# Kernel optimization log

Measured on AMD Instinct MI355X. Metric: run time of the kernel, lower is better.

## Reference

```python
import jax, jax.numpy as jnp
import numpy as np

B, T, F = 2048, 256, 64
EMB, UNITS = 16, 32
CAT = UNITS + EMB  # concat([h, x]) -> 48


def setup_inputs() -> dict:
    key = jax.random.key(0)
    ks = jax.random.split(key, 12)
    s = lambda k, shape, fan: jax.random.normal(k, shape, jnp.float32) / np.sqrt(fan)
    return {
        "x": jax.random.normal(ks[0], (B, T, F), jnp.float32),
        "W_emb": s(ks[1], (F, EMB), F), "b_emb": jnp.zeros((EMB,), jnp.float32),
        "W_f": s(ks[2], (CAT, UNITS), CAT), "b_f": jnp.zeros((UNITS,), jnp.float32),
        "W_i": s(ks[3], (CAT, UNITS), CAT), "b_i": jnp.zeros((UNITS,), jnp.float32),
        "W_c": s(ks[4], (CAT, UNITS), CAT), "b_c": jnp.zeros((UNITS,), jnp.float32),
        "W_o": s(ks[5], (CAT, UNITS), CAT), "b_o": jnp.zeros((UNITS,), jnp.float32),
        "W_out": s(ks[6], (UNITS, 1), UNITS), "b_out": jnp.zeros((1,), jnp.float32),
    }


def reference(x, W_emb, b_emb, W_f, b_f, W_i, b_i, W_c, b_c, W_o, b_o, W_out, b_out):
    # embedding: Dense(16, sigmoid)
    e = jax.nn.sigmoid(jnp.einsum('btf,fe->bte', x, W_emb) + b_emb)  # [B,T,EMB]
    e_t = jnp.swapaxes(e, 0, 1)  # [T,B,EMB] for scan

    h0 = jnp.zeros((x.shape[0], UNITS), jnp.float32)
    c0 = jnp.zeros((x.shape[0], UNITS), jnp.float32)

    # fuse 4 gate Dense layers into one GEMM per step (same math)
    W_gates = jnp.concatenate([W_f, W_i, W_c, W_o], axis=1)  # [CAT, 4*UNITS]
    b_gates = jnp.concatenate([b_f, b_i, b_c, b_o], axis=0)

    def step(carry, x_t):
        h, c = carry
        z = jnp.concatenate([h, x_t], axis=-1)  # concat([h_t, x_t])
        g = z @ W_gates + b_gates  # [B, 4*UNITS]
        f = jax.nn.sigmoid(g[:, :UNITS])
        i = jax.nn.sigmoid(g[:, UNITS:2 * UNITS])
        ch = jnp.tanh(g[:, 2 * UNITS:3 * UNITS])
        o = jax.nn.sigmoid(g[:, 3 * UNITS:])
        c_new = f * c + i * ch
        h_new = o * jnp.tanh(c_new)
        return (h_new, c_new), None

    (h_last, _), _ = jax.lax.scan(step, (h0, c0), e_t)
    return jax.nn.sigmoid(h_last @ W_out + b_out)  # [B,1]
```

## Files before the change

### kernel.cpp

```cpp
#include <hip/hip_runtime.h>

#define B_ 2048
#define T_ 256
#define F_ 64
#define EMB_ 16
#define UNITS_ 32
#define L2E 1.44269504f

typedef __attribute__((ext_vector_type(8))) short bf16x8;
typedef __attribute__((ext_vector_type(4))) float f32x4;

__device__ __forceinline__ unsigned short f2bf(float f) {
    unsigned u = __float_as_uint(f);
    return (unsigned short)((u + 0x7FFFu + ((u >> 16) & 1u)) >> 16);
}
__device__ __forceinline__ float fast_sigmoid(float x) {
    return __builtin_amdgcn_rcpf(1.0f + __builtin_amdgcn_exp2f(-L2E * x));
}

__global__ __launch_bounds__(64) void embed_mfma(
    const float* __restrict__ x, const float* __restrict__ Wemb,
    const float* __restrict__ bemb, unsigned int* __restrict__ e_ws)
{
    __shared__ unsigned short slab[2][16][72];

    const int lane = threadIdx.x;
    const int g = lane >> 4, c = lane & 15;
    const int tile = blockIdx.x >> 5;
    const int t0 = (blockIdx.x & 31) * 8;

    bf16x8 A1, A2;
    #pragma unroll
    for (int j = 0; j < 4; ++j) {
        A1[j]     = (short)f2bf(Wemb[(4 * g + j) * EMB_ + c]);
        A1[j + 4] = (short)f2bf(Wemb[(16 + 4 * g + j) * EMB_ + c]);
        A2[j]     = (short)f2bf(Wemb[(32 + 4 * g + j) * EMB_ + c]);
        A2[j + 4] = (short)f2bf(Wemb[(48 + 4 * g + j) * EMB_ + c]);
    }
    f32x4 bc;
    #pragma unroll
    for (int r = 0; r < 4; ++r) bc[r] = bemb[4 * g + r];

    const int sr = lane >> 2, sc = lane & 3;
    const float* xs = x + (size_t)(tile * 16 + sr) * T_ * F_ + sc * 16;

    float4 rld[4], nld[4];
    {
        const float4* p = (const float4*)(xs + (size_t)t0 * F_);
        rld[0] = p[0]; rld[1] = p[1]; rld[2] = p[2]; rld[3] = p[3];
    }

    #pragma unroll
    for (int i = 0; i < 9; ++i) {
        if (i < 7) {
            const float4* p = (const float4*)(xs + (size_t)(t0 + i + 1) * F_);
            nld[0] = p[0]; nld[1] = p[1]; nld[2] = p[2]; nld[3] = p[3];
        }
        if (i < 8) {
            const float* f = (const float*)rld;
            unsigned u[8];
            #pragma unroll
            for (int k = 0; k < 8; ++k)
                u[k] = (unsigned)f2bf(f[2 * k]) | ((unsigned)f2bf(f[2 * k + 1]) << 16);
            uint4* d = (uint4*)&slab[i & 1][sr][sc * 16];
            d[0] = make_uint4(u[0], u[1], u[2], u[3]);
            d[1] = make_uint4(u[4], u[5], u[6], u[7]);
        }
        if (i > 0) {
            const unsigned short* row = &slab[(i - 1) & 1][c][0];
            ushort4 l1 = *(const ushort4*)(row + 4 * g);
            ushort4 h1 = *(const ushort4*)(row + 16 + 4 * g);
            ushort4 l2 = *(const ushort4*)(row + 32 + 4 * g);
            ushort4 h2 = *(const ushort4*)(row + 48 + 4 * g);
            bf16x8 B1 = {(short)l1.x, (short)l1.y, (short)l1.z, (short)l1.w,
                         (short)h1.x, (short)h1.y, (short)h1.z, (short)h1.w};
            bf16x8 B2 = {(short)l2.x, (short)l2.y, (short)l2.z, (short)l2.w,
                         (short)h2.x, (short)h2.y, (short)h2.z, (short)h2.w};
            f32x4 acc = __builtin_amdgcn_mfma_f32_16x16x32_bf16(A1, B1, bc, 0, 0, 0);
            acc = __builtin_amdgcn_mfma_f32_16x16x32_bf16(A2, B2, acc, 0, 0, 0);
            unsigned u0 = (unsigned)f2bf(fast_sigmoid(acc[0])) |
                          ((unsigned)f2bf(fast_sigmoid(acc[1])) << 16);
            unsigned u1 = (unsigned)f2bf(fast_sigmoid(acc[2])) |
                          ((unsigned)f2bf(fast_sigmoid(acc[3])) << 16);
            size_t idx = (((size_t)tile * T_ + (t0 + i - 1)) * 64 + lane) * 2;
            *(uint2*)(e_ws + idx) = make_uint2(u0, u1);
        }
        #pragma unroll
        for (int k = 0; k < 4; ++k) rld[k] = nld[k];
    }
}

__global__ __launch_bounds__(256) void lstm_rec(
    const float* __restrict__ Wf, const float* __restrict__ bfv,
    const float* __restrict__ Wi, const float* __restrict__ biv,
    const float* __restrict__ Wc, const float* __restrict__ bcv,
    const float* __restrict__ Wo, const float* __restrict__ bov,
    const float* __restrict__ Wout, const float* __restrict__ bout,
    const unsigned int* __restrict__ e_ws, float* __restrict__ out)
{
    __shared__ unsigned short hx[2][16][36];
    __shared__ float pred[4][16];

    const int tid = threadIdx.x;
    const int w = tid >> 6;
    const int lane = tid & 63;
    const int g = lane >> 4, m15 = lane & 15;
    const int bt = blockIdx.x;

    const int gate = m15 & 3;
    const float* Wsel = (gate == 0) ? Wf : (gate == 1) ? Wi : (gate == 2) ? Wc : Wo;
    const float ascale = (gate == 2) ? (-2.0f * L2E) : (-L2E);
    const int uAb = 8 * w + 2 * (m15 >> 2);

    bf16x8 Ah[2], Ae[2];
    #pragma unroll
    for (int tau = 0; tau < 2; ++tau) {
        const int uA = uAb + tau;
        #pragma unroll
        for (int j = 0; j < 4; ++j) {
            Ah[tau][j]     = (short)f2bf(ascale * Wsel[(4 * g + j) * UNITS_ + uA]);
            Ah[tau][j + 4] = (short)f2bf(ascale * Wsel[(16 + 4 * g + j) * UNITS_ + uA]);
            Ae[tau][j]     = (short)f2bf(ascale * Wsel[(32 + 4 * g + j) * UNITS_ + uA]);
            Ae[tau][j + 4] = 0;
        }
    }
    f32x4 bias[2];
    #pragma unroll
    for (int tau = 0; tau < 2; ++tau) {
        const int u = 8 * w + 2 * g + tau;
        bias[tau][0] = -L2E * bfv[u];
        bias[tau][1] = -L2E * biv[u];
        bias[tau][2] = -2.0f * L2E * bcv[u];
        bias[tau][3] = -L2E * bov[u];
    }

    const uint2* ep = (const uint2*)e_ws + (size_t)bt * T_ * 64 + lane;
    uint2 ering[4];
    #pragma unroll
    for (int s = 0; s < 4; ++s) ering[s] = ep[(size_t)s * 64];

    for (int i = tid; i < 2 * 16 * 36 / 2; i += 256) ((unsigned*)hx)[i] = 0;
    __syncthreads();

    float c0 = 0.f, c1 = 0.f, hf0 = 0.f, hf1 = 0.f;

    auto cell = [&](const f32x4& acc, float& cst, float& hf) {
        float Ef = __builtin_amdgcn_exp2f(acc[0]);
        float Ei = __builtin_amdgcn_exp2f(acc[1]);
        float Ec = __builtin_amdgcn_exp2f(acc[2]);
        float Eo = __builtin_amdgcn_exp2f(acc[3]);
        float Pf = 1.f + Ef, Pi = 1.f + Ei, Pc = 1.f + Ec, Po = 1.f + Eo;
        float Mc = 1.f - Ec;
        float t1 = Pi * Pc;
        float num = fmaf(cst, t1, Pf * Mc);
        float den = Pf * t1;
        float cn = num * __builtin_amdgcn_rcpf(den);
        cst = cn;
        float Eh = __builtin_amdgcn_exp2f(cn * (-2.0f * L2E));
        float Mh = 1.f - Eh;
        float d2 = (1.f + Eh) * Po;
        hf = Mh * __builtin_amdgcn_rcpf(d2);
    };

    f32x4 Fe0, Fe1;
    {
        uint2 ev = ering[0];
        bf16x8 Be = {(short)(ev.x & 0xffff), (short)(ev.x >> 16),
                     (short)(ev.y & 0xffff), (short)(ev.y >> 16), 0, 0, 0, 0};
        Fe0 = __builtin_amdgcn_mfma_f32_16x16x32_bf16(Ae[0], Be, bias[0], 0, 0, 0);
        Fe1 = __builtin_amdgcn_mfma_f32_16x16x32_bf16(Ae[1], Be, bias[1], 0, 0, 0);
    }

    #pragma unroll 1
    for (int t = 0; t < T_; t += 4) {
        #pragma unroll
        for (int s = 0; s < 4; ++s) {
            const int u = t + s;
            const unsigned short* hrow = &hx[u & 1][m15][0];
            ushort4 hlo = *(const ushort4*)(hrow + 4 * g);
            ushort4 hhi = *(const ushort4*)(hrow + 16 + 4 * g);
            bf16x8 Bh = {(short)hlo.x, (short)hlo.y, (short)hlo.z, (short)hlo.w,
                         (short)hhi.x, (short)hhi.y, (short)hhi.z, (short)hhi.w};
            f32x4 a0 = __builtin_amdgcn_mfma_f32_16x16x32_bf16(Ah[0], Bh, Fe0, 0, 0, 0);
            f32x4 a1 = __builtin_amdgcn_mfma_f32_16x16x32_bf16(Ah[1], Bh, Fe1, 0, 0, 0);

            int tn = (u + 4 < T_) ? u + 4 : T_ - 1;
            uint2 ev = ering[(s + 1) & 3];
            ering[s] = ep[(size_t)tn * 64];
            bf16x8 Be = {(short)(ev.x & 0xffff), (short)(ev.x >> 16),
                         (short)(ev.y & 0xffff), (short)(ev.y >> 16), 0, 0, 0, 0};
            Fe0 = __builtin_amdgcn_mfma_f32_16x16x32_bf16(Ae[0], Be, bias[0], 0, 0, 0);
            Fe1 = __builtin_amdgcn_mfma_f32_16x16x32_bf16(Ae[1], Be, bias[1], 0, 0, 0);

            cell(a0, c0, hf0);
            cell(a1, c1, hf1);
            unsigned pk;
            asm("v_cvt_pk_bf16_f32 %0, %1, %2" : "=v"(pk) : "v"(hf0), "v"(hf1));
            *(unsigned*)&hx[(u + 1) & 1][m15][8 * w + 2 * g] = pk;

            asm volatile("s_waitcnt lgkmcnt(0)\n\ts_barrier" ::: "memory");
        }
    }

    float p = hf0 * Wout[8 * w + 2 * g] + hf1 * Wout[8 * w + 2 * g + 1];
    p += __shfl_xor(p, 16, 64);
    p += __shfl_xor(p, 32, 64);
    if (lane < 16) pred[w][lane] = p;
    __syncthreads();
    if (tid < 16)
        out[bt * 16 + tid] = fast_sigmoid(pred[0][tid] + pred[1][tid] +
                                          pred[2][tid] + pred[3][tid] + bout[0]);
}

extern "C" void kernel_launch(void* const* d_in, const int* in_sizes, int n_in,
                              void* d_out, int out_size, void* d_ws, size_t ws_size,
                              hipStream_t stream) {
    const float* x    = (const float*)d_in[0];
    const float* Wemb = (const float*)d_in[1];
    const float* bemb = (const float*)d_in[2];
    const float* Wf   = (const float*)d_in[3];
    const float* bfv  = (const float*)d_in[4];
    const float* Wi   = (const float*)d_in[5];
    const float* biv  = (const float*)d_in[6];
    const float* Wc   = (const float*)d_in[7];
    const float* bcv  = (const float*)d_in[8];
    const float* Wo   = (const float*)d_in[9];
    const float* bov  = (const float*)d_in[10];
    const float* Wout = (const float*)d_in[11];
    const float* bout = (const float*)d_in[12];
    float* out = (float*)d_out;
    unsigned int* e_ws = (unsigned int*)d_ws;

    hipLaunchKernelGGL(embed_mfma, dim3(128 * 32), dim3(64), 0, stream,
                       x, Wemb, bemb, e_ws);
    hipLaunchKernelGGL(lstm_rec, dim3(B_ / 16), dim3(256), 0, stream,
                       Wf, bfv, Wi, biv, Wc, bcv, Wo, bov, Wout, bout,
                       (const unsigned int*)e_ws, out);
}
```

Measured before the change: 88.37 us.

## Fuse embedding and recurrence into one kernel with per-chunk flag handoff

Merges the embedding GEMM kernel and the LSTM recurrence kernel into a single launch. The first 1024 blocks compute embedding chunks, one wave each, and publish a per-tile, per-chunk release flag. The last 128 blocks spin on those flags and consume chunks as they become ready. The goal is to overlap the recurrence with the embedding work and remove the gap between the two launches. The cost is that correctness depends on producer blocks being scheduled before or alongside consumers, which is a deadlock risk. It also relies on a magic-value flag protocol that is reset at the end, on workspace state that persists across calls, and on spin-wait overhead.

```diff
diff --git a/kernel.cpp b/kernel.cpp
--- a/kernel.cpp
+++ b/kernel.cpp
@@ -6,6 +6,7 @@
 #define EMB_ 16
 #define UNITS_ 32
 #define L2E 1.44269504f
+#define MAGIC 0x51E5C0DEu
 
 typedef __attribute__((ext_vector_type(8))) short bf16x8;
 typedef __attribute__((ext_vector_type(4))) float f32x4;
@@ -18,86 +19,18 @@
     return __builtin_amdgcn_rcpf(1.0f + __builtin_amdgcn_exp2f(-L2E * x));
 }
 
-__global__ __launch_bounds__(64) void embed_mfma(
-    const float* __restrict__ x, const float* __restrict__ Wemb,
-    const float* __restrict__ bemb, unsigned int* __restrict__ e_ws)
-{
-    __shared__ unsigned short slab[2][16][72];
-
-    const int lane = threadIdx.x;
-    const int g = lane >> 4, c = lane & 15;
-    const int tile = blockIdx.x >> 5;
-    const int t0 = (blockIdx.x & 31) * 8;
-
-    bf16x8 A1, A2;
-    #pragma unroll
-    for (int j = 0; j < 4; ++j) {
-        A1[j]     = (short)f2bf(Wemb[(4 * g + j) * EMB_ + c]);
-        A1[j + 4] = (short)f2bf(Wemb[(16 + 4 * g + j) * EMB_ + c]);
-        A2[j]     = (short)f2bf(Wemb[(32 + 4 * g + j) * EMB_ + c]);
-        A2[j + 4] = (short)f2bf(Wemb[(48 + 4 * g + j) * EMB_ + c]);
-    }
-    f32x4 bc;
-    #pragma unroll
-    for (int r = 0; r < 4; ++r) bc[r] = bemb[4 * g + r];
-
-    const int sr = lane >> 2, sc = lane & 3;
-    const float* xs = x + (size_t)(tile * 16 + sr) * T_ * F_ + sc * 16;
-
-    float4 rld[4], nld[4];
-    {
-        const float4* p = (const float4*)(xs + (size_t)t0 * F_);
-        rld[0] = p[0]; rld[1] = p[1]; rld[2] = p[2]; rld[3] = p[3];
-    }
-
-    #pragma unroll
-    for (int i = 0; i < 9; ++i) {
-        if (i < 7) {
-            const float4* p = (const float4*)(xs + (size_t)(t0 + i + 1) * F_);
-            nld[0] = p[0]; nld[1] = p[1]; nld[2] = p[2]; nld[3] = p[3];
-        }
-        if (i < 8) {
-            const float* f = (const float*)rld;
-            unsigned u[8];
-            #pragma unroll
-            for (int k = 0; k < 8; ++k)
-                u[k] = (unsigned)f2bf(f[2 * k]) | ((unsigned)f2bf(f[2 * k + 1]) << 16);
-            uint4* d = (uint4*)&slab[i & 1][sr][sc * 16];
-            d[0] = make_uint4(u[0], u[1], u[2], u[3]);
-            d[1] = make_uint4(u[4], u[5], u[6], u[7]);
-        }
-        if (i > 0) {
-            const unsigned short* row = &slab[(i - 1) & 1][c][0];
-            ushort4 l1 = *(const ushort4*)(row + 4 * g);
-            ushort4 h1 = *(const ushort4*)(row + 16 + 4 * g);
-            ushort4 l2 = *(const ushort4*)(row + 32 + 4 * g);
-            ushort4 h2 = *(const ushort4*)(row + 48 + 4 * g);
-            bf16x8 B1 = {(short)l1.x, (short)l1.y, (short)l1.z, (short)l1.w,
-                         (short)h1.x, (short)h1.y, (short)h1.z, (short)h1.w};
-            bf16x8 B2 = {(short)l2.x, (short)l2.y, (short)l2.z, (short)l2.w,
-                         (short)h2.x, (short)h2.y, (short)h2.z, (short)h2.w};
-            f32x4 acc = __builtin_amdgcn_mfma_f32_16x16x32_bf16(A1, B1, bc, 0, 0, 0);
-            acc = __builtin_amdgcn_mfma_f32_16x16x32_bf16(A2, B2, acc, 0, 0, 0);
-            unsigned u0 = (unsigned)f2bf(fast_sigmoid(acc[0])) |
-                          ((unsigned)f2bf(fast_sigmoid(acc[1])) << 16);
-            unsigned u1 = (unsigned)f2bf(fast_sigmoid(acc[2])) |
-                          ((unsigned)f2bf(fast_sigmoid(acc[3])) << 16);
-            size_t idx = (((size_t)tile * T_ + (t0 + i - 1)) * 64 + lane) * 2;
-            *(uint2*)(e_ws + idx) = make_uint2(u0, u1);
-        }
-        #pragma unroll
-        for (int k = 0; k < 4; ++k) rld[k] = nld[k];
-    }
-}
-
-__global__ __launch_bounds__(256) void lstm_rec(
+__global__ __launch_bounds__(256) void lstm_all(
+    const float* __restrict__ x,
+    const float* __restrict__ Wemb, const float* __restrict__ bemb,
     const float* __restrict__ Wf, const float* __restrict__ bfv,
     const float* __restrict__ Wi, const float* __restrict__ biv,
     const float* __restrict__ Wc, const float* __restrict__ bcv,
     const float* __restrict__ Wo, const float* __restrict__ bov,
     const float* __restrict__ Wout, const float* __restrict__ bout,
-    const unsigned int* __restrict__ e_ws, float* __restrict__ out)
+    unsigned int* __restrict__ e_ws, unsigned int* __restrict__ flags,
+    float* __restrict__ out)
 {
+    __shared__ unsigned short slab[4][2][16][72];
     __shared__ unsigned short hx[2][16][36];
     __shared__ float pred[4][16];
 
@@ -105,7 +38,80 @@
     const int w = tid >> 6;
     const int lane = tid & 63;
     const int g = lane >> 4, m15 = lane & 15;
-    const int bt = blockIdx.x;
+
+    if (blockIdx.x < 1024) {
+        const int id = blockIdx.x * 4 + w;
+        const int chunk = id >> 7;
+        const int tile = id & 127;
+        const int t0 = chunk * 8;
+
+        bf16x8 A1, A2;
+        #pragma unroll
+        for (int j = 0; j < 4; ++j) {
+            A1[j]     = (short)f2bf(Wemb[(4 * g + j) * EMB_ + m15]);
+            A1[j + 4] = (short)f2bf(Wemb[(16 + 4 * g + j) * EMB_ + m15]);
+            A2[j]     = (short)f2bf(Wemb[(32 + 4 * g + j) * EMB_ + m15]);
+            A2[j + 4] = (short)f2bf(Wemb[(48 + 4 * g + j) * EMB_ + m15]);
+        }
+        f32x4 bc;
+        #pragma unroll
+        for (int r = 0; r < 4; ++r) bc[r] = bemb[4 * g + r];
+
+        const int sr = lane >> 2, sc = lane & 3;
+        const float* xs = x + (size_t)(tile * 16 + sr) * T_ * F_ + sc * 16;
+
+        float4 rld[4], nld[4];
+        {
+            const float4* p = (const float4*)(xs + (size_t)t0 * F_);
+            rld[0] = p[0]; rld[1] = p[1]; rld[2] = p[2]; rld[3] = p[3];
+        }
+        #pragma unroll
+        for (int i = 0; i < 9; ++i) {
+            if (i < 7) {
+                const float4* p = (const float4*)(xs + (size_t)(t0 + i + 1) * F_);
+                nld[0] = p[0]; nld[1] = p[1]; nld[2] = p[2]; nld[3] = p[3];
+            }
+            if (i < 8) {
+                const float* f = (const float*)rld;
+                unsigned u[8];
+                #pragma unroll
+                for (int k = 0; k < 8; ++k)
+                    u[k] = (unsigned)f2bf(f[2 * k]) | ((unsigned)f2bf(f[2 * k + 1]) << 16);
+                uint4* d = (uint4*)&slab[w][i & 1][sr][sc * 16];
+                d[0] = make_uint4(u[0], u[1], u[2], u[3]);
+                d[1] = make_uint4(u[4], u[5], u[6], u[7]);
+            }
+            if (i > 0) {
+                const unsigned short* row = &slab[w][(i - 1) & 1][m15][0];
+                ushort4 l1 = *(const ushort4*)(row + 4 * g);
+                ushort4 h1 = *(const ushort4*)(row + 16 + 4 * g);
+                ushort4 l2 = *(const ushort4*)(row + 32 + 4 * g);
+                ushort4 h2 = *(const ushort4*)(row + 48 + 4 * g);
+                bf16x8 B1 = {(short)l1.x, (short)l1.y, (short)l1.z, (short)l1.w,
+                             (short)h1.x, (short)h1.y, (short)h1.z, (short)h1.w};
+                bf16x8 B2 = {(short)l2.x, (short)l2.y, (short)l2.z, (short)l2.w,
+                             (short)h2.x, (short)h2.y, (short)h2.z, (short)h2.w};
+                f32x4 acc = __builtin_amdgcn_mfma_f32_16x16x32_bf16(A1, B1, bc, 0, 0, 0);
+                acc = __builtin_amdgcn_mfma_f32_16x16x32_bf16(A2, B2, acc, 0, 0, 0);
+                unsigned u0 = (unsigned)f2bf(fast_sigmoid(acc[0])) |
+                              ((unsigned)f2bf(fast_sigmoid(acc[1])) << 16);
+                unsigned u1 = (unsigned)f2bf(fast_sigmoid(acc[2])) |
+                              ((unsigned)f2bf(fast_sigmoid(acc[3])) << 16);
+                size_t idx = (((size_t)tile * T_ + (t0 + i - 1)) * 64 + lane) * 2;
+                *(uint2*)(e_ws + idx) = make_uint2(u0, u1);
+            }
+            #pragma unroll
+            for (int k = 0; k < 4; ++k) rld[k] = nld[k];
+        }
+        asm volatile("s_waitcnt vmcnt(0)" ::: "memory");
+        if (lane == 0)
+            __hip_atomic_store(&flags[tile * 32 + chunk], MAGIC,
+                               __ATOMIC_RELEASE, __HIP_MEMORY_SCOPE_AGENT);
+        return;
+    }
+
+    const int bt = blockIdx.x - 1024;
+    unsigned int* flagp = flags + bt * 32;
 
     const int gate = m15 & 3;
     const float* Wsel = (gate == 0) ? Wf : (gate == 1) ? Wi : (gate == 2) ? Wc : Wo;
@@ -133,6 +139,13 @@
         bias[tau][2] = -2.0f * L2E * bcv[u];
         bias[tau][3] = -L2E * bov[u];
     }
+
+    unsigned fut;
+    do {
+        fut = __hip_atomic_load(flagp, __ATOMIC_ACQUIRE, __HIP_MEMORY_SCOPE_AGENT);
+        if (fut != MAGIC) __builtin_amdgcn_s_sleep(1);
+    } while (fut != MAGIC);
+    fut = __hip_atomic_load(flagp + 1, __ATOMIC_ACQUIRE, __HIP_MEMORY_SCOPE_AGENT);
 
     const uint2* ep = (const uint2*)e_ws + (size_t)bt * T_ * 64 + lane;
     uint2 ering[4];
@@ -161,12 +174,14 @@
         float d2 = (1.f + Eh) * Po;
         hf = Mh * __builtin_amdgcn_rcpf(d2);
     };
+    auto mkBe = [](uint2 ev) -> bf16x8 {
+        return bf16x8{(short)(ev.x & 0xffff), (short)(ev.x >> 16),
+                      (short)(ev.y & 0xffff), (short)(ev.y >> 16), 0, 0, 0, 0};
+    };
 
     f32x4 Fe0, Fe1;
     {
-        uint2 ev = ering[0];
-        bf16x8 Be = {(short)(ev.x & 0xffff), (short)(ev.x >> 16),
-                     (short)(ev.y & 0xffff), (short)(ev.y >> 16), 0, 0, 0, 0};
+        bf16x8 Be = mkBe(ering[0]);
         Fe0 = __builtin_amdgcn_mfma_f32_16x16x32_bf16(Ae[0], Be, bias[0], 0, 0, 0);
         Fe1 = __builtin_amdgcn_mfma_f32_16x16x32_bf16(Ae[1], Be, bias[1], 0, 0, 0);
     }
@@ -185,10 +200,20 @@
             f32x4 a1 = __builtin_amdgcn_mfma_f32_16x16x32_bf16(Ah[1], Bh, Fe1, 0, 0, 0);
 
             int tn = (u + 4 < T_) ? u + 4 : T_ - 1;
+            if ((tn & 7) == 0) {
+                const int c = tn >> 3;
+                while (fut != MAGIC) {
+                    __builtin_amdgcn_s_sleep(1);
+                    fut = __hip_atomic_load(flagp + c, __ATOMIC_ACQUIRE,
+                                            __HIP_MEMORY_SCOPE_AGENT);
+                }
+                fut = (c < 31) ? __hip_atomic_load(flagp + c + 1, __ATOMIC_ACQUIRE,
+                                                   __HIP_MEMORY_SCOPE_AGENT)
+                               : MAGIC;
+            }
             uint2 ev = ering[(s + 1) & 3];
             ering[s] = ep[(size_t)tn * 64];
-            bf16x8 Be = {(short)(ev.x & 0xffff), (short)(ev.x >> 16),
-                         (short)(ev.y & 0xffff), (short)(ev.y >> 16), 0, 0, 0, 0};
+            bf16x8 Be = mkBe(ev);
             Fe0 = __builtin_amdgcn_mfma_f32_16x16x32_bf16(Ae[0], Be, bias[0], 0, 0, 0);
             Fe1 = __builtin_amdgcn_mfma_f32_16x16x32_bf16(Ae[1], Be, bias[1], 0, 0, 0);
 
@@ -201,6 +226,9 @@
             asm volatile("s_waitcnt lgkmcnt(0)\n\ts_barrier" ::: "memory");
         }
     }
+
+    asm volatile("s_waitcnt vmcnt(0)" ::: "memory");
+    if (tid < 32) flagp[tid] = 0u;
 
     float p = hf0 * Wout[8 * w + 2 * g] + hf1 * Wout[8 * w + 2 * g + 1];
     p += __shfl_xor(p, 16, 64);
@@ -229,11 +257,10 @@
     const float* Wout = (const float*)d_in[11];
     const float* bout = (const float*)d_in[12];
     float* out = (float*)d_out;
-    unsigned int* e_ws = (unsigned int*)d_ws;
-
-    hipLaunchKernelGGL(embed_mfma, dim3(128 * 32), dim3(64), 0, stream,
-                       x, Wemb, bemb, e_ws);
-    hipLaunchKernelGGL(lstm_rec, dim3(B_ / 16), dim3(256), 0, stream,
-                       Wf, bfv, Wi, biv, Wc, bcv, Wo, bov, Wout, bout,
-                       (const unsigned int*)e_ws, out);
-}
+    unsigned int* e_ws  = (unsigned int*)d_ws;
+    unsigned int* flags = e_ws + (16u << 20) / 4;
+
+    hipLaunchKernelGGL(lstm_all, dim3(1024 + 128), dim3(256), 0, stream,
+                       x, Wemb, bemb, Wf, bfv, Wi, biv, Wc, bcv, Wo, bov,
+                       Wout, bout, e_ws, flags, out);
+}
```

Measured after the change: 237.0 us. +168.2%, slower.

## Split LSTM recurrence across 8 waves with one hidden unit per lane

Applied to the files above, without the earlier changes.

Doubles the recurrence block from 4 to 8 waves, so each wave computes 4 hidden units instead of 8. Each lane now issues one recurrent MFMA and one input-projection MFMA per step, and evaluates one cell instead of two. This shortens the per-step critical path of the serial scan. The cost is a barrier across 8 waves every step, 16-bit LDS stores in place of packed 32-bit ones, and a redundant duplicate load of the e stream in each wave.

```diff
diff --git a/kernel.cpp b/kernel.cpp
--- a/kernel.cpp
+++ b/kernel.cpp
@@ -90,7 +90,7 @@
     }
 }
 
-__global__ __launch_bounds__(256) void lstm_rec(
+__global__ __launch_bounds__(512) void lstm_rec(
     const float* __restrict__ Wf, const float* __restrict__ bfv,
     const float* __restrict__ Wi, const float* __restrict__ biv,
     const float* __restrict__ Wc, const float* __restrict__ bcv,
@@ -99,7 +99,7 @@
     const unsigned int* __restrict__ e_ws, float* __restrict__ out)
 {
     __shared__ unsigned short hx[2][16][36];
-    __shared__ float pred[4][16];
+    __shared__ float pred[8][16];
 
     const int tid = threadIdx.x;
     const int w = tid >> 6;
@@ -110,41 +110,34 @@
     const int gate = m15 & 3;
     const float* Wsel = (gate == 0) ? Wf : (gate == 1) ? Wi : (gate == 2) ? Wc : Wo;
     const float ascale = (gate == 2) ? (-2.0f * L2E) : (-L2E);
-    const int uAb = 8 * w + 2 * (m15 >> 2);
-
-    bf16x8 Ah[2], Ae[2];
-    #pragma unroll
-    for (int tau = 0; tau < 2; ++tau) {
-        const int uA = uAb + tau;
-        #pragma unroll
-        for (int j = 0; j < 4; ++j) {
-            Ah[tau][j]     = (short)f2bf(ascale * Wsel[(4 * g + j) * UNITS_ + uA]);
-            Ah[tau][j + 4] = (short)f2bf(ascale * Wsel[(16 + 4 * g + j) * UNITS_ + uA]);
-            Ae[tau][j]     = (short)f2bf(ascale * Wsel[(32 + 4 * g + j) * UNITS_ + uA]);
-            Ae[tau][j + 4] = 0;
-        }
-    }
-    f32x4 bias[2];
-    #pragma unroll
-    for (int tau = 0; tau < 2; ++tau) {
-        const int u = 8 * w + 2 * g + tau;
-        bias[tau][0] = -L2E * bfv[u];
-        bias[tau][1] = -L2E * biv[u];
-        bias[tau][2] = -2.0f * L2E * bcv[u];
-        bias[tau][3] = -L2E * bov[u];
-    }
+    const int uA = 4 * w + (m15 >> 2);
+
+    bf16x8 Ah, Ae;
+    #pragma unroll
+    for (int j = 0; j < 4; ++j) {
+        Ah[j]     = (short)f2bf(ascale * Wsel[(4 * g + j) * UNITS_ + uA]);
+        Ah[j + 4] = (short)f2bf(ascale * Wsel[(16 + 4 * g + j) * UNITS_ + uA]);
+        Ae[j]     = (short)f2bf(ascale * Wsel[(32 + 4 * g + j) * UNITS_ + uA]);
+        Ae[j + 4] = 0;
+    }
+    const int cu = 4 * w + g;
+    f32x4 bias;
+    bias[0] = -L2E * bfv[cu];
+    bias[1] = -L2E * biv[cu];
+    bias[2] = -2.0f * L2E * bcv[cu];
+    bias[3] = -L2E * bov[cu];
 
     const uint2* ep = (const uint2*)e_ws + (size_t)bt * T_ * 64 + lane;
     uint2 ering[4];
     #pragma unroll
     for (int s = 0; s < 4; ++s) ering[s] = ep[(size_t)s * 64];
 
-    for (int i = tid; i < 2 * 16 * 36 / 2; i += 256) ((unsigned*)hx)[i] = 0;
+    for (int i = tid; i < 2 * 16 * 36 / 2; i += 512) ((unsigned*)hx)[i] = 0;
     __syncthreads();
 
-    float c0 = 0.f, c1 = 0.f, hf0 = 0.f, hf1 = 0.f;
-
-    auto cell = [&](const f32x4& acc, float& cst, float& hf) {
+    float cst = 0.f, hf = 0.f;
+
+    auto cell = [&](const f32x4& acc) {
         float Ef = __builtin_amdgcn_exp2f(acc[0]);
         float Ei = __builtin_amdgcn_exp2f(acc[1]);
         float Ec = __builtin_amdgcn_exp2f(acc[2]);
@@ -161,14 +154,15 @@
         float d2 = (1.f + Eh) * Po;
         hf = Mh * __builtin_amdgcn_rcpf(d2);
     };
-
-    f32x4 Fe0, Fe1;
+    auto mkBe = [](uint2 ev) -> bf16x8 {
+        return bf16x8{(short)(ev.x & 0xffff), (short)(ev.x >> 16),
+                      (short)(ev.y & 0xffff), (short)(ev.y >> 16), 0, 0, 0, 0};
+    };
+
+    f32x4 Fe;
     {
-        uint2 ev = ering[0];
-        bf16x8 Be = {(short)(ev.x & 0xffff), (short)(ev.x >> 16),
-                     (short)(ev.y & 0xffff), (short)(ev.y >> 16), 0, 0, 0, 0};
-        Fe0 = __builtin_amdgcn_mfma_f32_16x16x32_bf16(Ae[0], Be, bias[0], 0, 0, 0);
-        Fe1 = __builtin_amdgcn_mfma_f32_16x16x32_bf16(Ae[1], Be, bias[1], 0, 0, 0);
+        bf16x8 Be = mkBe(ering[0]);
+        Fe = __builtin_amdgcn_mfma_f32_16x16x32_bf16(Ae, Be, bias, 0, 0, 0);
     }
 
     #pragma unroll 1
@@ -181,35 +175,32 @@
             ushort4 hhi = *(const ushort4*)(hrow + 16 + 4 * g);
             bf16x8 Bh = {(short)hlo.x, (short)hlo.y, (short)hlo.z, (short)hlo.w,
                          (short)hhi.x, (short)hhi.y, (short)hhi.z, (short)hhi.w};
-            f32x4 a0 = __builtin_amdgcn_mfma_f32_16x16x32_bf16(Ah[0], Bh, Fe0, 0, 0, 0);
-            f32x4 a1 = __builtin_amdgcn_mfma_f32_16x16x32_bf16(Ah[1], Bh, Fe1, 0, 0, 0);
+            f32x4 acc = __builtin_amdgcn_mfma_f32_16x16x32_bf16(Ah, Bh, Fe, 0, 0, 0);
 
             int tn = (u + 4 < T_) ? u + 4 : T_ - 1;
             uint2 ev = ering[(s + 1) & 3];
             ering[s] = ep[(size_t)tn * 64];
-            bf16x8 Be = {(short)(ev.x & 0xffff), (short)(ev.x >> 16),
-                         (short)(ev.y & 0xffff), (short)(ev.y >> 16), 0, 0, 0, 0};
-            Fe0 = __builtin_amdgcn_mfma_f32_16x16x32_bf16(Ae[0], Be, bias[0], 0, 0, 0);
-            Fe1 = __builtin_amdgcn_mfma_f32_16x16x32_bf16(Ae[1], Be, bias[1], 0, 0, 0);
-
-            cell(a0, c0, hf0);
-            cell(a1, c1, hf1);
-            unsigned pk;
-            asm("v_cvt_pk_bf16_f32 %0, %1, %2" : "=v"(pk) : "v"(hf0), "v"(hf1));
-            *(unsigned*)&hx[(u + 1) & 1][m15][8 * w + 2 * g] = pk;
+            bf16x8 Be = mkBe(ev);
+            Fe = __builtin_amdgcn_mfma_f32_16x16x32_bf16(Ae, Be, bias, 0, 0, 0);
+
+            cell(acc);
+            hx[(u + 1) & 1][m15][cu] = f2bf(hf);
 
             asm volatile("s_waitcnt lgkmcnt(0)\n\ts_barrier" ::: "memory");
         }
     }
 
-    float p = hf0 * Wout[8 * w + 2 * g] + hf1 * Wout[8 * w + 2 * g + 1];
+    float p = hf * Wout[cu];
     p += __shfl_xor(p, 16, 64);
     p += __shfl_xor(p, 32, 64);
     if (lane < 16) pred[w][lane] = p;
     __syncthreads();
-    if (tid < 16)
-        out[bt * 16 + tid] = fast_sigmoid(pred[0][tid] + pred[1][tid] +
-                                          pred[2][tid] + pred[3][tid] + bout[0]);
+    if (tid < 16) {
+        float sum = bout[0];
+        #pragma unroll
+        for (int ww = 0; ww < 8; ++ww) sum += pred[ww][tid];
+        out[bt * 16 + tid] = fast_sigmoid(sum);
+    }
 }
 
 extern "C" void kernel_launch(void* const* d_in, const int* in_sizes, int n_in,
@@ -233,7 +224,7 @@
 
     hipLaunchKernelGGL(embed_mfma, dim3(128 * 32), dim3(64), 0, stream,
                        x, Wemb, bemb, e_ws);
-    hipLaunchKernelGGL(lstm_rec, dim3(B_ / 16), dim3(256), 0, stream,
+    hipLaunchKernelGGL(lstm_rec, dim3(B_ / 16), dim3(512), 0, stream,
                        Wf, bfv, Wi, biv, Wc, bcv, Wo, bov, Wout, bout,
                        (const unsigned int*)e_ws, out);
 }
```

Result: no change. 89.90 us (+1.7%).
